# Kernel tuning notes

Measured on AMD Instinct MI355X. Metric: run time of the kernel, lower is better.

Reference implementation:

```python
import jax, jax.numpy as jnp
import numpy as np

DIM = 384
HEADS = 12
K = 3          # kernel_size
PAD = 1
STRIDE = 1
B, H, W = 8, 56, 56


def conv1x1(x, w, b=None):
    # x: [B,C,H,W], w: [O,C]
    y = jnp.einsum('bchw,oc->bohw', x, w)
    if b is not None:
        y = y + b[None, :, None, None]
    return y


def unfold(x, k, p, s):
    # torch nn.Unfold: returns patches [B, C, k*k, nH, nW], kernel row-major, channel-major overall
    Bx, C, Hx, Wx = x.shape
    nH = (Hx + 2 * p - k) // s + 1
    nW = (Wx + 2 * p - k) // s + 1
    xp = jnp.pad(x, ((0, 0), (0, 0), (p, p), (p, p)))
    cols = [xp[:, :, i:i + s * nH:s, j:j + s * nW:s] for i in range(k) for j in range(k)]
    return jnp.stack(cols, axis=2), nH, nW


def fold(col, Hx, Wx, k, p, s):
    # torch F.fold (col2im): scatter-add overlapping windows. col: [B, C, k*k, nH, nW]
    Bx, C, _, nH, nW = col.shape
    canvas = jnp.zeros((Bx, C, Hx + 2 * p, Wx + 2 * p), col.dtype)
    idx = 0
    for i in range(k):
        for j in range(k):
            canvas = canvas.at[:, :, i:i + s * nH:s, j:j + s * nW:s].add(col[:, :, idx])
            idx += 1
    return canvas[:, :, p:p + Hx, p:p + Wx]


def setup_inputs() -> dict:
    key = jax.random.key(0)
    ks = jax.random.split(key, 5)
    k2 = K * K
    x = jax.random.normal(ks[0], (B, DIM, H, W), dtype=jnp.float32)
    v_w = jax.random.normal(ks[1], (DIM, DIM), dtype=jnp.float32) * 0.02
    v_b = jnp.zeros((DIM,), dtype=jnp.float32)
    attn_w = jax.random.normal(ks[2], (k2 * k2 * HEADS, DIM), dtype=jnp.float32) * 0.02
    proj_w = jax.random.normal(ks[3], (DIM, DIM), dtype=jnp.float32) * 0.02
    return {'x': x, 'v_w': v_w, 'v_b': v_b, 'attn_w': attn_w, 'proj_w': proj_w}


def reference(x, v_w, v_b, attn_w, proj_w):
    Bx, C, Hx, Wx = x.shape
    k2 = K * K
    hd = C // HEADS  # head dim
    # value projection + unfold into overlapping k x k windows
    v = conv1x1(x, v_w, v_b)
    vcol, nH, nW = unfold(v, K, PAD, STRIDE)        # [B, C, k2, nH, nW]
    L = nH * nW
    v = vcol.reshape(Bx, HEADS, hd, k2, L)          # split C = (heads, hd), heads slow
    v = v.transpose(0, 1, 4, 3, 2)                  # [B, n, L, k2(d), hd]
    # adaptive avg pool to (nH, nW); with stride=1 this is identity (pool window 1)
    ph, pw = Hx // nH, Wx // nW
    xp = x.reshape(Bx, C, nH, ph, nW, pw).mean(axis=(3, 5))
    # per-pixel attention logits, channel layout = ((i*k2 + d)*HEADS + head)
    a = jnp.einsum('bchw,oc->bohw', xp, attn_w)     # [B, k2*k2*n, nH, nW]
    a = a.reshape(Bx, k2, k2, HEADS, L)             # [B, i, d, n, L]
    a = a.transpose(0, 3, 4, 1, 2)                  # [B, n, L, i, d]
    a = jax.nn.softmax(a, axis=-1)
    out = jnp.einsum('bnlid,bnldh->bnlih', a, v)    # [B, n, L, i, hd]
    out = out.transpose(0, 1, 4, 3, 2)              # [B, n, hd, i, L] -> channel (n*hd+h)
    out = out.reshape(Bx, C, k2, nH, nW)
    out = fold(out, Hx, Wx, K, PAD, STRIDE)         # scatter-add windows back
    return conv1x1(out, proj_w)
```

## Files before the change

kernel.cpp:

```cpp
#include <hip/hip_runtime.h>
#include <hip/hip_bf16.h>

#define DIM   384
#define HEADS 12
#define K2    9
#define HH    56
#define WW    56
#define HWP   3136
#define BB    8
#define AO    972
#define AOP   1024
#define MCAT  1408
#define PP    3200
#define PPAD  3600
#define W60   60

#define WBLK     2688
#define HALOBLK  696

typedef __hip_bfloat16 bf16;
typedef short bf16x8 __attribute__((ext_vector_type(8)));
typedef short bf16x4v __attribute__((ext_vector_type(4)));
typedef float f32x4 __attribute__((ext_vector_type(4)));
typedef float f32x2 __attribute__((ext_vector_type(2)));

static __device__ __forceinline__ float b2f(bf16 v) { return __bfloat162float(v); }
static __device__ __forceinline__ float bs2f(short s) {
    return __uint_as_float(((unsigned int)(unsigned short)s) << 16);
}
static __device__ __forceinline__ short f2bs(float f) {
    __hip_bfloat16 h = __float2bfloat16(f);
    return *(short*)&h;
}
static __device__ __forceinline__ f32x2 unpk(unsigned int u) {
    f32x2 r;
    r[0] = __uint_as_float(u << 16);
    r[1] = __uint_as_float(u & 0xffff0000u);
    return r;
}

static __device__ __forceinline__ void gl_lds16(const bf16* g, bf16* l) {
    __builtin_amdgcn_global_load_lds(
        (const __attribute__((address_space(1))) unsigned int*)g,
        (__attribute__((address_space(3))) unsigned int*)l, 16, 0, 0);
}

__global__ __launch_bounds__(256) void prep_kernel(
        const float* __restrict__ x, const float* __restrict__ v_w,
        const float* __restrict__ attn_w, const float* __restrict__ proj_w,
        bf16* __restrict__ xT, bf16* __restrict__ wcat, bf16* __restrict__ wp,
        bf16* __restrict__ vP) {
    const int bid = blockIdx.x;
    if (bid < 400) {
        const int lane = threadIdx.x & 63, w = threadIdx.x >> 6;
        const int p = (bid % 50) * 64 + lane;
        const int b = bid / 50;
        bf16* dst = xT + ((size_t)b * PP + p) * DIM;
        if (p >= HWP) {
            bf16x8 z = {};
            for (int cg = w; cg < 48; cg += 4) *(bf16x8*)(dst + cg * 8) = z;
            return;
        }
        const float* src = x + (size_t)b * DIM * HWP + p;
        for (int cg = w; cg < 48; cg += 4) {
            bf16x8 v;
#pragma unroll
            for (int j = 0; j < 8; j++) v[j] = f2bs(src[(size_t)(cg * 8 + j) * HWP]);
            *(bf16x8*)(dst + cg * 8) = v;
        }
    } else if (bid < 400 + WBLK) {
        const int idx = (bid - 400) * 256 + threadIdx.x;
        const int NCAT = MCAT * DIM;
        if (idx < NCAT) {
            const int row = idx / DIM, col = idx % DIM;
            float v;
            if (row < 384) v = v_w[row * DIM + col];
            else { const int r2 = row - 384; v = (r2 < AO) ? attn_w[r2 * DIM + col] : 0.f; }
            *(short*)&wcat[idx] = f2bs(v);
        } else {
            const int j = idx - NCAT;
            if (j < 384 * DIM) *(short*)&wp[j] = f2bs(proj_w[j]);
        }
    } else {
        const int hidx = (bid - 400 - WBLK) * 256 + threadIdx.x;
        const int b = hidx / 22272;
        const int r = hidx % 22272;
        const int hp = r / 48, cgi = r % 48;
        int row, col;
        if (hp < 240) {
            const int rr = hp / 60;
            row = (rr < 2) ? rr : rr + 56;
            col = hp % 60;
        } else {
            const int h2 = hp - 240;
            row = 2 + (h2 >> 2);
            const int c4 = h2 & 3;
            col = (c4 < 2) ? c4 : c4 + 56;
        }
        bf16x8 z = {};
        *(bf16x8*)(vP + ((size_t)b * PPAD + row * W60 + col) * DIM + cgi * 8) = z;
    }
}

#define GEMM_MAIN_LOOP_V4(Ab, Bb, lA, lB, acc)                                 \
    for (int k0 = 0; k0 < DIM; k0 += 64) {                                     \
        _Pragma("unroll")                                                      \
        for (int r = 0; r < 4; r++) {                                          \
            int idx = r * 256 + t;                                             \
            int row = idx >> 3;                                                \
            int kq = ((idx & 7) - (row >> 1)) & 7;                             \
            gl_lds16(Ab + (size_t)row * DIM + k0 + kq * 8, lA + idx * 8);      \
        }                                                                      \
        _Pragma("unroll")                                                      \
        for (int r = 0; r < 4; r++) {                                          \
            int idx = r * 256 + t;                                             \
            int row = idx >> 3;                                                \
            int kq = ((idx & 7) - (row >> 1)) & 7;                             \
            gl_lds16(Bb + (size_t)row * DIM + k0 + kq * 8, lB + idx * 8);      \
        }                                                                      \
        __syncthreads();                                                       \
        _Pragma("unroll")                                                      \
        for (int h = 0; h < 2; h++) {                                          \
            const int swzh = (((h << 2) + quad + (l16 >> 1)) & 7) * 8;         \
            bf16x8 af[4], bfr[4];                                              \
            _Pragma("unroll")                                                  \
            for (int mt = 0; mt < 4; mt++)                                     \
                af[mt] = *(const bf16x8*)(lA + (wm * 64 + mt * 16 + l16) * 64 + swzh); \
            _Pragma("unroll")                                                  \
            for (int nt = 0; nt < 4; nt++)                                     \
                bfr[nt] = *(const bf16x8*)(lB + (wn * 64 + nt * 16 + l16) * 64 + swzh); \
            _Pragma("unroll")                                                  \
            for (int mt = 0; mt < 4; mt++)                                     \
                _Pragma("unroll")                                              \
                for (int nt = 0; nt < 4; nt++)                                 \
                    acc[mt][nt] = __builtin_amdgcn_mfma_f32_16x16x32_bf16(     \
                        af[mt], bfr[nt], acc[mt][nt], 0, 0, 0);                \
        }                                                                      \
        __syncthreads();                                                       \
    }

__global__ __launch_bounds__(256) void gemm12_kernel(
        const bf16* __restrict__ A, const bf16* __restrict__ Bt,
        const float* __restrict__ bias, bf16* __restrict__ vP,
        bf16* __restrict__ lT) {
    __shared__ bf16 lds[16384];
    bf16* lA = lds;
    bf16* lB = lds + 8192;
    const int t = threadIdx.x;
    const int lane = t & 63, w = t >> 6;
    const int wm = w & 1, wn = w >> 1;
    const int quad = lane >> 4, l16 = lane & 15;
    const int n0 = blockIdx.x * 128;
    const int m0 = blockIdx.y * 128;
    const int b = blockIdx.z;

    const bf16* Ab = A + (size_t)m0 * DIM;
    const bf16* Bb = Bt + ((size_t)b * PP + n0) * DIM;

    f32x4 acc[4][4] = {};
    GEMM_MAIN_LOOP_V4(Ab, Bb, lA, lB, acc)

    const bool isv = (m0 < 384);
    const int ch0 = isv ? m0 : m0 - 384;

    bf16* wbuf = lds + w * 1152;
    const int nr = lane >> 2;
    const int mc = (lane & 3) * 16;
#pragma unroll
    for (int nt = 0; nt < 4; nt++) {
#pragma unroll
        for (int mt = 0; mt < 4; mt++) {
            float4 bi = make_float4(0.f, 0.f, 0.f, 0.f);
            if (isv) bi = *(const float4*)(bias + ch0 + wm * 64 + mt * 16 + quad * 4);
            bf16x4v pk;
            pk[0] = f2bs(acc[mt][nt][0] + bi.x);
            pk[1] = f2bs(acc[mt][nt][1] + bi.y);
            pk[2] = f2bs(acc[mt][nt][2] + bi.z);
            pk[3] = f2bs(acc[mt][nt][3] + bi.w);
            *(bf16x4v*)(wbuf + l16 * 72 + mt * 16 + quad * 4) = pk;
        }
        bf16x8 v0 = *(const bf16x8*)(wbuf + nr * 72 + mc);
        bf16x8 v1 = *(const bf16x8*)(wbuf + nr * 72 + mc + 8);
        const int p = n0 + wn * 64 + nt * 16 + nr;
        if (p < HWP) {
            bf16* dp;
            if (isv) {
                const int y = p / WW;
                dp = vP + ((size_t)b * PPAD + p + y * 4 + 122) * DIM + ch0 + wm * 64 + mc;
            } else {
                dp = lT + ((size_t)b * PP + p) * AOP + ch0 + wm * 64 + mc;
            }
            *(bf16x8*)dp = v0;
            *(bf16x8*)(dp + 8) = v1;
        }
    }
}

__global__ __launch_bounds__(256) void gemm_planar_kernel(
        const bf16* __restrict__ A, const bf16* __restrict__ Bt,
        float* __restrict__ out) {
    __shared__ bf16 lds[16384];
    bf16* lA = lds;
    bf16* lB = lds + 8192;
    const int t = threadIdx.x;
    const int lane = t & 63, w = t >> 6;
    const int wm = w & 1, wn = w >> 1;
    const int quad = lane >> 4, l16 = lane & 15;
    const int n0 = blockIdx.x * 128;
    const int m0 = blockIdx.y * 128;
    const int b = blockIdx.z;

    const bf16* Ab = A + (size_t)m0 * DIM;
    const bf16* Bb = Bt + ((size_t)b * PP + n0) * DIM;

    f32x4 acc[4][4] = {};
    GEMM_MAIN_LOOP_V4(Ab, Bb, lA, lB, acc)

#pragma unroll
    for (int mt = 0; mt < 4; mt++) {
#pragma unroll
        for (int nt = 0; nt < 4; nt++) {
            int p = n0 + wn * 64 + nt * 16 + l16;
            if (p >= HWP) continue;
#pragma unroll
            for (int reg = 0; reg < 4; reg++) {
                int o = m0 + wm * 64 + mt * 16 + quad * 4 + reg;
                out[((size_t)b * DIM + o) * HWP + p] = acc[mt][nt][reg];
            }
        }
    }
}

__global__ __launch_bounds__(384) void attn_fold_kernel(
        const bf16* __restrict__ lT, const bf16* __restrict__ vP,
        bf16* __restrict__ cT) {
    __shared__ bf16 P[8 * 9 * 12 * 9];
    __shared__ float Wf[8 * 25 * 12];
    const int t = threadIdx.x;
    const int b = blockIdx.y;
    const int pix0 = blockIdx.x * 8;
    const int Y = pix0 / WW, X0 = pix0 % WW;

    for (int r = t; r < 864; r += 384) {
        const int px = r / 108, rem = r % 108;
        const int i = rem / 12, n = rem % 12;
        const int ir = i / 3, ic = i % 3;
        const int yi = Y + 1 - ir, xi = X0 + px + 1 - ic;
        bf16* Pd = &P[r * 9];
        if (yi < 0 || yi >= HH || xi < 0 || xi >= WW) {
#pragma unroll
            for (int d = 0; d < K2; d++) *(short*)&Pd[d] = 0;
        } else {
            const bf16* base = lT + ((size_t)b * PP + yi * WW + xi) * AOP + i * 108 + n;
            float lv[K2];
            float m = -1e30f;
#pragma unroll
            for (int d = 0; d < K2; d++) {
                lv[d] = b2f(base[d * 12]);
                m = fmaxf(m, lv[d]);
            }
            float s = 0.f;
#pragma unroll
            for (int d = 0; d < K2; d++) { lv[d] = __expf(lv[d] - m); s += lv[d]; }
            const float inv = 1.f / s;
#pragma unroll
            for (int d = 0; d < K2; d++) *(short*)&Pd[d] = f2bs(lv[d] * inv);
        }
    }
    __syncthreads();

    if (t < 300) {
        const int off = t / 12, n = t % 12;
        const int dy = off / 5 - 2, dx = off % 5 - 2;
        const int ir_lo = max(0, -dy), ir_hi = min(2, 2 - dy);
        const int ic_lo = max(0, -dx), ic_hi = min(2, 2 - dx);
#pragma unroll
        for (int px = 0; px < 8; px++) {
            float wsum = 0.f;
            for (int ir = ir_lo; ir <= ir_hi; ir++)
                for (int ic = ic_lo; ic <= ic_hi; ic++) {
                    const int i = ir * 3 + ic;
                    const int d = (dy + ir) * 3 + (dx + ic);
                    wsum += b2f(P[((px * 9 + i) * 12 + n) * 9 + d]);
                }
            Wf[(px * 25 + off) * 12 + n] = wsum;
        }
    }
    __syncthreads();

    const int px = t / 48, cg = t % 48;
    const int X = X0 + px;
    const int n = cg >> 2;
    const float* Wp = &Wf[px * 300 + n];
    const bf16* vbp = vP + ((size_t)b * PPAD + (size_t)(Y + 2) * W60 + (X + 2)) * DIM + cg * 8;
    f32x2 a2[4] = {};
#pragma unroll
    for (int dy = -2; dy <= 2; dy++) {
        const bf16* rowb = vbp + dy * (W60 * DIM);
        const float* wrow = Wp + (dy + 2) * 60;
#pragma unroll
        for (int dx = -2; dx <= 2; dx++) {
            const float w = wrow[(dx + 2) * 12];
            const uint4 d = *(const uint4*)(rowb + dx * DIM);
            f32x2 w2; w2[0] = w; w2[1] = w;
            a2[0] = __builtin_elementwise_fma(unpk(d.x), w2, a2[0]);
            a2[1] = __builtin_elementwise_fma(unpk(d.y), w2, a2[1]);
            a2[2] = __builtin_elementwise_fma(unpk(d.z), w2, a2[2]);
            a2[3] = __builtin_elementwise_fma(unpk(d.w), w2, a2[3]);
        }
    }
    bf16x8 po;
#pragma unroll
    for (int j = 0; j < 4; j++) {
        po[2 * j]     = f2bs(a2[j][0]);
        po[2 * j + 1] = f2bs(a2[j][1]);
    }
    *(bf16x8*)(cT + ((size_t)b * PP + pix0 + px) * DIM + cg * 8) = po;
}

extern "C" void kernel_launch(void* const* d_in, const int* in_sizes, int n_in,
                              void* d_out, int out_size, void* d_ws, size_t ws_size,
                              hipStream_t stream) {
    const float* x      = (const float*)d_in[0];
    const float* v_w    = (const float*)d_in[1];
    const float* v_b    = (const float*)d_in[2];
    const float* attn_w = (const float*)d_in[3];
    const float* proj_w = (const float*)d_in[4];
    float* out = (float*)d_out;

    bf16* xT    = (bf16*)d_ws;
    bf16* vP    = xT + (size_t)BB * PP * DIM;
    bf16* lT    = vP + (size_t)BB * PPAD * DIM;
    bf16* wcat  = lT + (size_t)BB * PP * AOP;
    bf16* wp    = wcat + (size_t)MCAT * DIM;
    bf16* cT    = xT;

    const int nprep = 400 + WBLK + HALOBLK;
    prep_kernel<<<nprep, 256, 0, stream>>>(x, v_w, attn_w, proj_w, xT, wcat, wp, vP);

    gemm12_kernel<<<dim3(PP / 128, MCAT / 128, BB), 256, 0, stream>>>(wcat, xT, v_b, vP, lT);
    attn_fold_kernel<<<dim3(HWP / 8, BB), 384, 0, stream>>>(lT, vP, cT);
    gemm_planar_kernel<<<dim3(PP / 128, 3, BB), 256, 0, stream>>>(wp, cT, out);
}
```

Baseline: 217.4 us.

## Swizzle block order across XCDs and shrink logit row padding

The GEMM launches become 1D grids whose block index is remapped so that consecutive blocks, which land round-robin on the 8 XCDs, go to the same batch and N-tile. This lets each XCD's L2 reuse the A and B tiles. The attention kernel interleaves the batch index into blockIdx.x for the same reason. The logit row stride drops from 1024 to 976, which cuts write and read traffic for the lT buffer, and a channel bound check is added so the last M tile does not write past the row. The trade-off is extra index arithmetic and reliance on the hardware's round-robin block dispatch.

```diff
diff --git a/kernel.cpp b/kernel.cpp
--- a/kernel.cpp
+++ b/kernel.cpp
@@ -9,7 +9,7 @@
 #define HWP   3136
 #define BB    8
 #define AO    972
-#define AOP   1024
+#define AOP   976
 #define MCAT  1408
 #define PP    3200
 #define PPAD  3600
@@ -150,9 +150,15 @@
     const int lane = t & 63, w = t >> 6;
     const int wm = w & 1, wn = w >> 1;
     const int quad = lane >> 4, l16 = lane & 15;
-    const int n0 = blockIdx.x * 128;
-    const int m0 = blockIdx.y * 128;
-    const int b = blockIdx.z;
+
+    const int bid = blockIdx.x;
+    const int swz = (bid & 7) * 275 + (bid >> 3);
+    const int mtile = swz % 11;
+    const int nb = swz / 11;
+    const int ntile = nb % 25;
+    const int b = nb / 25;
+    const int n0 = ntile * 128;
+    const int m0 = mtile * 128;
 
     const bf16* Ab = A + (size_t)m0 * DIM;
     const bf16* Bb = Bt + ((size_t)b * PP + n0) * DIM;
@@ -182,13 +188,14 @@
         bf16x8 v0 = *(const bf16x8*)(wbuf + nr * 72 + mc);
         bf16x8 v1 = *(const bf16x8*)(wbuf + nr * 72 + mc + 8);
         const int p = n0 + wn * 64 + nt * 16 + nr;
-        if (p < HWP) {
+        const int cc = ch0 + wm * 64 + mc;
+        if (p < HWP && (isv || cc < AOP)) {
             bf16* dp;
             if (isv) {
                 const int y = p / WW;
-                dp = vP + ((size_t)b * PPAD + p + y * 4 + 122) * DIM + ch0 + wm * 64 + mc;
+                dp = vP + ((size_t)b * PPAD + p + y * 4 + 122) * DIM + cc;
             } else {
-                dp = lT + ((size_t)b * PP + p) * AOP + ch0 + wm * 64 + mc;
+                dp = lT + ((size_t)b * PP + p) * AOP + cc;
             }
             *(bf16x8*)dp = v0;
             *(bf16x8*)(dp + 8) = v1;
@@ -206,9 +213,15 @@
     const int lane = t & 63, w = t >> 6;
     const int wm = w & 1, wn = w >> 1;
     const int quad = lane >> 4, l16 = lane & 15;
-    const int n0 = blockIdx.x * 128;
-    const int m0 = blockIdx.y * 128;
-    const int b = blockIdx.z;
+
+    const int bid = blockIdx.x;
+    const int swz = (bid & 7) * 75 + (bid >> 3);
+    const int mtile = swz % 3;
+    const int nb = swz / 3;
+    const int ntile = nb % 25;
+    const int b = nb / 25;
+    const int n0 = ntile * 128;
+    const int m0 = mtile * 128;
 
     const bf16* Ab = A + (size_t)m0 * DIM;
     const bf16* Bb = Bt + ((size_t)b * PP + n0) * DIM;
@@ -237,8 +250,8 @@
     __shared__ bf16 P[8 * 9 * 12 * 9];
     __shared__ float Wf[8 * 25 * 12];
     const int t = threadIdx.x;
-    const int b = blockIdx.y;
-    const int pix0 = blockIdx.x * 8;
+    const int b = blockIdx.x & 7;
+    const int pix0 = (blockIdx.x >> 3) * 8;
     const int Y = pix0 / WW, X0 = pix0 % WW;
 
     for (int r = t; r < 864; r += 384) {
@@ -338,7 +351,7 @@
     const int nprep = 400 + WBLK + HALOBLK;
     prep_kernel<<<nprep, 256, 0, stream>>>(x, v_w, attn_w, proj_w, xT, wcat, wp, vP);
 
-    gemm12_kernel<<<dim3(PP / 128, MCAT / 128, BB), 256, 0, stream>>>(wcat, xT, v_b, vP, lT);
-    attn_fold_kernel<<<dim3(HWP / 8, BB), 384, 0, stream>>>(lT, vP, cT);
-    gemm_planar_kernel<<<dim3(PP / 128, 3, BB), 256, 0, stream>>>(wp, cT, out);
-}
+    gemm12_kernel<<<2200, 256, 0, stream>>>(wcat, xT, v_b, vP, lT);
+    attn_fold_kernel<<<3136, 384, 0, stream>>>(lT, vP, cT);
+    gemm_planar_kernel<<<600, 256, 0, stream>>>(wp, cT, out);
+}
```

Measured after the change: 204.7 us. -5.8%, faster.
